# Optimization experiments

Measured on AMD Instinct MI355X. Metric: run time of the kernel, lower is better.

## Reference

```python
import jax, jax.numpy as jnp
import numpy as np

B, T, N, K = 1024, 4096, 2048, 16
M = 1 << K  # per-neuron memory size (use_hashing=False -> 2**k)


def setup_inputs() -> dict:
    key = jax.random.key(0)
    k1, k2, k3 = jax.random.split(key, 3)
    input_bits = jax.random.randint(k1, (B, T), 0, 2, dtype=jnp.int32)          # 0/1 bits
    connections = jax.random.randint(k2, (N, K), 0, T, dtype=jnp.int32)         # fixed wiring
    memory = jax.random.randint(k3, (N, M), 0, 256, dtype=jnp.int32)            # per-neuron RAM contents
    return {"input_bits": input_bits, "connections": connections, "memory": memory}


def reference(input_bits, connections, memory):
    # gather the k wired bits for every neuron: [B, N, K]
    gathered = input_bits[:, connections].astype(jnp.int32)
    # bit weights = powers of two (RAMNeuron._bit_weights), LSB-first
    bit_weights = (jnp.int32(1) << jnp.arange(K, dtype=jnp.int32))              # [K]
    # weighted sum -> memory address per (sample, neuron): [B, N]
    addresses = jnp.sum(gathered * bit_weights, axis=-1)
    # per-neuron memory lookup: memory[n, addresses[b, n]] -> [B, N]
    mems = memory[jnp.arange(N)[None, :], addresses]
    # output is the stored LSB as a bool bit
    return (mems & 1).astype(jnp.bool_)
```

## Files before the change

kernel.cpp:

```cpp
#include <hip/hip_runtime.h>
#include <cstdint>

#define Bc 1024
#define Tc 4096
#define Nc 2048
#define Kc 16
#define Mc 65536

__global__ __launch_bounds__(256) void ram_lookup_fused(
    const int* __restrict__ input_bits,
    const int* __restrict__ connections,
    const int* __restrict__ memory,
    int* __restrict__ out)
{
    __shared__ uint32_t bits[Tc / 32];

    const int b    = blockIdx.x;
    const int tid  = threadIdx.x;
    const int lane = tid & 63;
    const int wave = tid >> 6;

    const int* row = input_bits + (size_t)b * Tc;

#pragma unroll
    for (int i = 0; i < Tc / 256; ++i) {
        const int pos = i * 256 + wave * 64 + lane;
        const unsigned long long m = __ballot(row[pos] & 1);
        if (lane == 0) {
            const int w64 = i * 4 + wave;
            bits[w64 * 2]     = (uint32_t)m;
            bits[w64 * 2 + 1] = (uint32_t)(m >> 32);
        }
    }
    __syncthreads();

    int vals[Nc / 256];
#pragma unroll
    for (int i = 0; i < Nc / 256; ++i) {
        const int n = i * 256 + tid;
        const int4* cp = (const int4*)(connections + n * Kc);
        const int4 c0 = cp[0], c1 = cp[1], c2 = cp[2], c3 = cp[3];
        const int c[16] = {c0.x, c0.y, c0.z, c0.w,
                           c1.x, c1.y, c1.z, c1.w,
                           c2.x, c2.y, c2.z, c2.w,
                           c3.x, c3.y, c3.z, c3.w};
        uint32_t a = 0;
#pragma unroll
        for (int k = 0; k < 16; ++k) {
            const uint32_t t = (uint32_t)c[k];
            a |= ((bits[t >> 5] >> (t & 31)) & 1u) << k;
        }
        vals[i] = __builtin_nontemporal_load(memory + ((size_t)n << 16) + a);
    }

#pragma unroll
    for (int i = 0; i < Nc / 256; ++i) {
        __builtin_nontemporal_store(vals[i] & 1,
                                    out + (size_t)b * Nc + i * 256 + tid);
    }
}

extern "C" void kernel_launch(void* const* d_in, const int* in_sizes, int n_in,
                              void* d_out, int out_size, void* d_ws, size_t ws_size,
                              hipStream_t stream) {
    const int* input_bits  = (const int*)d_in[0];
    const int* connections = (const int*)d_in[1];
    const int* memory      = (const int*)d_in[2];
    int* out               = (int*)d_out;

    hipLaunchKernelGGL(ram_lookup_fused, dim3(Bc), dim3(256), 0, stream,
                       input_bits, connections, memory, out);
}
```

Baseline: 616.1 us.

## Pre-pack memory LSBs into a bit table before the lookup

Adds a streaming pre-pass that reads the whole int32 memory and uses wave ballots to pack only bit 0 of each entry into a bitmap in workspace. That table is 32x smaller than the original memory. The lookup kernel then does its random accesses against this compact table, which is more likely to stay in cache, instead of issuing scattered 4-byte loads into the large array. The cost is a full sequential read of the memory array on every call plus a second kernel launch. It falls back to the original kernel when the workspace is too small.

Measured after the change: 737.3 us. 19.7% more time.

```diff
diff --git a/kernel.cpp b/kernel.cpp
--- a/kernel.cpp
+++ b/kernel.cpp
@@ -6,6 +6,88 @@
 #define Nc 2048
 #define Kc 16
 #define Mc 65536
+
+#define PACK_GRID 2048
+#define PACK_BLK  256
+
+__global__ __launch_bounds__(PACK_BLK) void pack_bit0(
+    const int* __restrict__ memory,
+    unsigned long long* __restrict__ packed)
+{
+    const int tid  = threadIdx.x;
+    const int lane = tid & 63;
+    const size_t stride = (size_t)PACK_GRID * PACK_BLK;
+    size_t base = (size_t)blockIdx.x * PACK_BLK + tid;
+
+    for (int it = 0; it < 256 / 8; ++it) {
+        int v[8];
+#pragma unroll
+        for (int j = 0; j < 8; ++j)
+            v[j] = __builtin_nontemporal_load(memory + base + (size_t)j * stride);
+#pragma unroll
+        for (int j = 0; j < 8; ++j) {
+            const unsigned long long m = __ballot(v[j] & 1);
+            if (lane == 0) {
+                packed[(base + (size_t)j * stride) >> 6] = m;
+            }
+        }
+        base += 8 * stride;
+    }
+}
+
+__global__ __launch_bounds__(256) void ram_lookup_packed(
+    const int* __restrict__ input_bits,
+    const int* __restrict__ connections,
+    const uint32_t* __restrict__ packed,
+    int* __restrict__ out)
+{
+    __shared__ uint32_t bits[Tc / 32];
+
+    const int b    = blockIdx.x;
+    const int tid  = threadIdx.x;
+    const int lane = tid & 63;
+    const int wave = tid >> 6;
+
+    const int* row = input_bits + (size_t)b * Tc;
+
+#pragma unroll
+    for (int i = 0; i < Tc / 256; ++i) {
+        const int pos = i * 256 + wave * 64 + lane;
+        const unsigned long long m = __ballot(row[pos] & 1);
+        if (lane == 0) {
+            const int w64 = i * 4 + wave;
+            bits[w64 * 2]     = (uint32_t)m;
+            bits[w64 * 2 + 1] = (uint32_t)(m >> 32);
+        }
+    }
+    __syncthreads();
+
+    int vals[Nc / 256];
+#pragma unroll
+    for (int i = 0; i < Nc / 256; ++i) {
+        const int n = i * 256 + tid;
+        const int4* cp = (const int4*)(connections + n * Kc);
+        const int4 c0 = cp[0], c1 = cp[1], c2 = cp[2], c3 = cp[3];
+        const int c[16] = {c0.x, c0.y, c0.z, c0.w,
+                           c1.x, c1.y, c1.z, c1.w,
+                           c2.x, c2.y, c2.z, c2.w,
+                           c3.x, c3.y, c3.z, c3.w};
+        uint32_t a = 0;
+#pragma unroll
+        for (int k = 0; k < 16; ++k) {
+            const uint32_t t = (uint32_t)c[k];
+            a |= ((bits[t >> 5] >> (t & 31)) & 1u) << k;
+        }
+        const uint32_t w = packed[((uint32_t)n << 11) + (a >> 5)];
+        vals[i] = (int)((w >> (a & 31)) & 1u);
+    }
+
+#pragma unroll
+    for (int i = 0; i < Nc / 256; ++i) {
+        __builtin_nontemporal_store(vals[i],
+                                    out + (size_t)b * Nc + i * 256 + tid);
+    }
+}
 
 __global__ __launch_bounds__(256) void ram_lookup_fused(
     const int* __restrict__ input_bits,
@@ -68,6 +150,16 @@
     const int* memory      = (const int*)d_in[2];
     int* out               = (int*)d_out;
 
-    hipLaunchKernelGGL(ram_lookup_fused, dim3(Bc), dim3(256), 0, stream,
-                       input_bits, connections, memory, out);
+    const size_t packed_bytes = (size_t)Nc * Mc / 8;
+
+    if (ws_size >= packed_bytes) {
+        unsigned long long* packed64 = (unsigned long long*)d_ws;
+        hipLaunchKernelGGL(pack_bit0, dim3(PACK_GRID), dim3(PACK_BLK), 0, stream,
+                           memory, packed64);
+        hipLaunchKernelGGL(ram_lookup_packed, dim3(Bc), dim3(256), 0, stream,
+                           input_bits, connections, (const uint32_t*)d_ws, out);
+    } else {
+        hipLaunchKernelGGL(ram_lookup_fused, dim3(Bc), dim3(256), 0, stream,
+                           input_bits, connections, memory, out);
+    }
 }
```
